# Optimization experiments

Hardware: AMD Instinct MI355X
Metric: run time of the kernel (lower is better)

Reference implementation:

```python
import jax, jax.numpy as jnp
import numpy as np

B, T, D, H = 4, 2048, 1024, 16
HD = D // H

def setup_inputs() -> dict:
    key = jax.random.key(0)
    ks = jax.random.split(key, 7)
    s = 1.0 / np.sqrt(D)
    return {
        "x": jax.random.normal(ks[0], (B, T, D), dtype=jnp.float32),
        "w_qkv": jax.random.uniform(ks[1], (D, 3 * D), jnp.float32, -s, s),
        "b_qkv": jax.random.uniform(ks[2], (3 * D,), jnp.float32, -s, s),
        "w_proj": jax.random.uniform(ks[3], (D, D), jnp.float32, -s, s),
        "b_proj": jax.random.uniform(ks[4], (D,), jnp.float32, -s, s),
        "ln_gamma": jnp.ones((D,), jnp.float32),
        "ln_beta": jnp.zeros((D,), jnp.float32),
    }

def reference(x, w_qkv, b_qkv, w_proj, b_proj, ln_gamma, ln_beta):
    eps = 1e-5
    scale = HD ** -0.5
    residual = x
    # Pre-norm LayerNorm over last dim
    mu = jnp.mean(x, axis=-1, keepdims=True)
    var = jnp.mean(jnp.square(x - mu), axis=-1, keepdims=True)
    xn = (x - mu) * jax.lax.rsqrt(var + eps) * ln_gamma + ln_beta
    # QKV projection: (B,T,3D) -> (3,B,H,T,HD)
    qkv = xn @ w_qkv + b_qkv
    qkv = qkv.reshape(B, T, 3, H, HD).transpose(2, 0, 3, 1, 4)
    q, k, v = qkv[0], qkv[1], qkv[2]
    # Scaled dot-product attention (full T x T scores, as in source)
    attn = jnp.einsum('bhqd,bhkd->bhqk', q, k) * scale
    attn = jax.nn.softmax(attn, axis=-1)
    out = jnp.einsum('bhqk,bhkd->bhqd', attn, v)
    out = out.transpose(0, 2, 1, 3).reshape(B, T, D)
    out = out @ w_proj + b_proj
    return residual + out
```

## Files before the change

kernel.cpp:

```cpp
#include <hip/hip_runtime.h>
#include <cstdint>
#include <cstddef>

#define B_ 4
#define T_ 2048
#define D_ 1024
#define H_ 16

typedef __attribute__((ext_vector_type(8))) short short8;
typedef __attribute__((ext_vector_type(4))) float f32x4;
typedef __attribute__((ext_vector_type(8))) unsigned short u16x8;

__device__ __forceinline__ unsigned short f2b16(float f) {
  union { float f; unsigned int u; } un; un.f = f;
  unsigned int r = un.u + 0x7fffu + ((un.u >> 16) & 1u);
  return (unsigned short)(r >> 16);
}
__device__ __forceinline__ void async_cp16(const void* g, void* l) {
  __builtin_amdgcn_global_load_lds((const __attribute__((address_space(1))) void*)g,
                                   (__attribute__((address_space(3))) void*)l,
                                   16, 0, 0);
}
__device__ __forceinline__ f32x4 mfma16(short8 a, short8 b, f32x4 c) {
  return __builtin_amdgcn_mfma_f32_16x16x32_bf16(a, b, c, 0, 0, 0);
}

__global__ __launch_bounds__(256) void prep_kernel(const float* __restrict__ x,
                                                   const float* __restrict__ gamma,
                                                   const float* __restrict__ beta,
                                                   unsigned short* __restrict__ xn,
                                                   const float* __restrict__ wq,
                                                   unsigned short* __restrict__ wTq,
                                                   const float* __restrict__ wp,
                                                   unsigned short* __restrict__ wTp) {
  __shared__ float sh[8];
  __shared__ float tile[32][33];
  const int bid = blockIdx.x;
  const int t = threadIdx.x;

  if (bid < 8192) {
    const int row = bid;
    const float4 v = ((const float4*)(x + (size_t)row * D_))[t];
    float s  = v.x + v.y + v.z + v.w;
    float s2 = v.x*v.x + v.y*v.y + v.z*v.z + v.w*v.w;
    #pragma unroll
    for (int off = 32; off > 0; off >>= 1) {
      s  += __shfl_down(s, off);
      s2 += __shfl_down(s2, off);
    }
    const int wv = t >> 6, lane = t & 63;
    if (lane == 0) { sh[wv] = s; sh[4 + wv] = s2; }
    __syncthreads();
    if (t == 0) {
      float ts  = sh[0] + sh[1] + sh[2] + sh[3];
      float ts2 = sh[4] + sh[5] + sh[6] + sh[7];
      float mu  = ts * (1.0f / D_);
      float var = ts2 * (1.0f / D_) - mu * mu;
      sh[0] = mu;
      sh[1] = rsqrtf(var + 1e-5f);
    }
    __syncthreads();
    const float mu = sh[0], rs = sh[1];
    const float4 g  = ((const float4*)gamma)[t];
    const float4 bb = ((const float4*)beta)[t];
    ushort4 o;
    o.x = f2b16((v.x - mu) * rs * g.x + bb.x);
    o.y = f2b16((v.y - mu) * rs * g.y + bb.y);
    o.z = f2b16((v.z - mu) * rs * g.z + bb.z);
    o.w = f2b16((v.w - mu) * rs * g.w + bb.w);
    ((ushort4*)(xn + (size_t)row * D_))[t] = o;
  } else {
    const float* w; unsigned short* wT; int K, N, bx, by;
    if (bid < 8192 + 3072) {
      const int idx = bid - 8192;
      w = wq; wT = wTq; K = 1024; N = 3072; bx = idx % 96; by = idx / 96;
    } else {
      const int idx = bid - 11264;
      w = wp; wT = wTp; K = 1024; N = 1024; bx = idx % 32; by = idx / 32;
    }
    const int n0 = bx * 32, k0 = by * 32;
    const int tx = t & 31, ty = t >> 5;
    #pragma unroll
    for (int i = 0; i < 32; i += 8)
      tile[ty + i][tx] = w[(size_t)(k0 + ty + i) * N + n0 + tx];
    __syncthreads();
    #pragma unroll
    for (int i = 0; i < 32; i += 8)
      wT[(size_t)(n0 + ty + i) * K + k0 + tx] = f2b16(tile[tx][ty + i]);
  }
}

__global__ __launch_bounds__(512, 2) void gemm256_qkv(const unsigned short* __restrict__ A,
                                                      const unsigned short* __restrict__ Bt,
                                                      const float* __restrict__ bias,
                                                      unsigned short* __restrict__ qB,
                                                      unsigned short* __restrict__ kB,
                                                      unsigned short* __restrict__ vtB) {
  constexpr int K = 1024;
  constexpr int NT = K / 64;
  __shared__ __align__(16) unsigned short As[32768];
  __shared__ __align__(16) unsigned short Bs[32768];

  const int tid  = threadIdx.x;
  const int lane = tid & 63;
  const int wv   = tid >> 6;
  const int l15  = lane & 15, quad = lane >> 4;
  const int wr   = wv >> 1;
  const int wc   = wv & 1;

  const int w = (blockIdx.x & 7) * 48 + (blockIdx.x >> 3);
  const int tileM = (w & 31) * 256;
  const int tileN = (w >> 5) * 256;

  const int sr  = tid >> 3;
  const int scs = ((tid & 7) ^ (sr & 7)) * 8;
  const unsigned short* gA = A  + (size_t)(tileM + sr) * K + scs;
  const unsigned short* gB = Bt + (size_t)(tileN + sr) * K + scs;

  auto stageA = [&](int h, int ko, int wbuf) {
    const unsigned short* g = gA + (size_t)(h * 128) * K + ko;
    unsigned short* l = &As[wbuf * 16384 + h * 8192 + tid * 8];
    async_cp16(g, l);
    async_cp16(g + (size_t)64 * K, l + 4096);
  };
  auto stageB = [&](int h, int ko, int wbuf) {
    const unsigned short* g = gB + (size_t)(h * 128) * K + ko;
    unsigned short* l = &Bs[wbuf * 16384 + h * 8192 + tid * 8];
    async_cp16(g, l);
    async_cp16(g + (size_t)64 * K, l + 4096);
  };

  const int rA  = wr * 32 + l15;
  const int rB  = wc * 64 + l15;
  const int ck0 = ((0 + quad) ^ (l15 & 7)) * 8;
  const int ck1 = ((4 + quad) ^ (l15 & 7)) * 8;

  f32x4 acc[2][2][2][4] = {};

#define MFMA16(QM, QN, AF, BF)                                                          \
  do {                                                                                  \
    _Pragma("unroll") for (int fm = 0; fm < 2; ++fm)                                    \
    _Pragma("unroll") for (int fn = 0; fn < 4; ++fn) {                                  \
      acc[QM][QN][fm][fn] = mfma16(AF[fm][0], BF[fn][0], acc[QM][QN][fm][fn]);          \
      acc[QM][QN][fm][fn] = mfma16(AF[fm][1], BF[fn][1], acc[QM][QN][fm][fn]);          \
    }                                                                                   \
  } while (0)

  stageA(0, 0, 0);
  stageB(0, 0, 0);
  stageB(1, 0, 0);
  stageA(1, 0, 0);
  asm volatile("s_waitcnt vmcnt(4)" ::: "memory");
  asm volatile("s_barrier" ::: "memory");

  #pragma unroll 2
  for (int kt = 0; kt < NT; ++kt) {
    const int buf = kt & 1;
    const unsigned short* Ab = &As[buf * 16384];
    const unsigned short* Bb = &Bs[buf * 16384];
    const int wbuf = buf ^ 1;
    const bool st = (kt + 1) < NT;
    const int ko = (kt + 1) * 64;

    short8 a[2][2], b0[4][2], b1[4][2];

    #pragma unroll
    for (int fm = 0; fm < 2; ++fm) {
      a[fm][0] = *(const short8*)&Ab[(rA + fm * 16) * 64 + ck0];
      a[fm][1] = *(const short8*)&Ab[(rA + fm * 16) * 64 + ck1];
    }
    #pragma unroll
    for (int fn = 0; fn < 4; ++fn) {
      b0[fn][0] = *(const short8*)&Bb[(rB + fn * 16) * 64 + ck0];
      b0[fn][1] = *(const short8*)&Bb[(rB + fn * 16) * 64 + ck1];
    }
    if (st) stageA(0, ko, wbuf);
    asm volatile("s_waitcnt lgkmcnt(0)" ::: "memory");
    __builtin_amdgcn_sched_barrier(0);
    __builtin_amdgcn_s_setprio(1);
    MFMA16(0, 0, a, b0);
    __builtin_amdgcn_s_setprio(0);
    if (st) asm volatile("s_waitcnt vmcnt(4)" ::: "memory");
    else    asm volatile("s_waitcnt vmcnt(2)" ::: "memory");
    asm volatile("s_barrier" ::: "memory");

    #pragma unroll
    for (int fn = 0; fn < 4; ++fn) {
      b1[fn][0] = *(const short8*)&Bb[8192 + (rB + fn * 16) * 64 + ck0];
      b1[fn][1] = *(const short8*)&Bb[8192 + (rB + fn * 16) * 64 + ck1];
    }
    if (st) stageB(0, ko, wbuf);
    asm volatile("s_waitcnt lgkmcnt(0)" ::: "memory");
    __builtin_amdgcn_sched_barrier(0);
    __builtin_amdgcn_s_setprio(1);
    MFMA16(0, 1, a, b1);
    __builtin_amdgcn_s_setprio(0);
    if (st) asm volatile("s_waitcnt vmcnt(4)" ::: "memory");
    else    asm volatile("s_waitcnt vmcnt(0)" ::: "memory");
    asm volatile("s_barrier" ::: "memory");

    #pragma unroll
    for (int fm = 0; fm < 2; ++fm) {
      a[fm][0] = *(const short8*)&Ab[8192 + (rA + fm * 16) * 64 + ck0];
      a[fm][1] = *(const short8*)&Ab[8192 + (rA + fm * 16) * 64 + ck1];
    }
    if (st) stageB(1, ko, wbuf);
    asm volatile("s_waitcnt lgkmcnt(0)" ::: "memory");
    __builtin_amdgcn_sched_barrier(0);
    __builtin_amdgcn_s_setprio(1);
    MFMA16(1, 0, a, b0);
    __builtin_amdgcn_s_setprio(0);
    asm volatile("s_barrier" ::: "memory");

    if (st) stageA(1, ko, wbuf);
    __builtin_amdgcn_s_setprio(1);
    MFMA16(1, 1, a, b1);
    __builtin_amdgcn_s_setprio(0);
    if (st) asm volatile("s_waitcnt vmcnt(4)" ::: "memory");
    asm volatile("s_barrier" ::: "memory");
  }
#undef MFMA16

  if (tileN < 2048) {
    unsigned short* E = &As[wv * 2304];
    #pragma unroll
    for (int qm = 0; qm < 2; ++qm) {
      #pragma unroll
      for (int qn = 0; qn < 2; ++qn) {
        const int colBase = tileN + qn * 128 + wc * 64;
        const int rowBase = tileM + qm * 128 + wr * 32;
        #pragma unroll
        for (int fn = 0; fn < 4; ++fn) {
          const int col = colBase + fn * 16 + l15;
          const float bv = bias[col];
          const float sc = (col < 1024) ? 0.180336880f : 1.0f;
          #pragma unroll
          for (int fm = 0; fm < 2; ++fm)
            #pragma unroll
            for (int r = 0; r < 4; ++r)
              E[(fm * 16 + quad * 4 + r) * 72 + fn * 16 + l15] =
                  f2b16((acc[qm][qn][fm][fn][r] + bv) * sc);
        }
        const int secq = colBase >> 10;
        const int hh   = (colBase & 1023) >> 6;
        unsigned short* outSec = (secq == 0) ? qB : kB;
        #pragma unroll
        for (int it = 0; it < 4; ++it) {
          const int lrow = it * 8 + (lane >> 3);
          const int row = rowBase + lrow;
          const int b_ = row >> 11, tt = row & 2047;
          const u16x8 val = *(const u16x8*)&E[lrow * 72 + (lane & 7) * 8];
          *(u16x8*)(outSec + ((size_t)(b_ * 16 + hh) * T_ + tt) * 64 + (lane & 7) * 8) = val;
        }
      }
    }
  } else {
    const int b_    = tileM >> 11;
    const int tbase = tileM & 2047;
    const int h0    = (tileN - 2048) >> 6;
    unsigned short* TL = (wr < 2) ? As : Bs;
    const int cpr = 32 * (wr & 1) + 8 * quad;
    #pragma unroll
    for (int qm = 0; qm < 2; ++qm) {
      #pragma unroll
      for (int qn = 0; qn < 2; ++qn) {
        const int head = qn * 2 + wc;
        const int colBase = tileN + qn * 128 + wc * 64;
        #pragma unroll
        for (int fn = 0; fn < 4; ++fn) {
          const int dv = fn * 16 + l15;
          const float bv = bias[colBase + fn * 16 + l15];
          #pragma unroll
          for (int fm = 0; fm < 2; ++fm)
            #pragma unroll
            for (int r = 0; r < 4; ++r)
              TL[head * 4352 + dv * 68 + cpr + 4 * fm + r] =
                  f2b16(acc[qm][qn][fm][fn][r] + bv);
        }
      }
      __syncthreads();
      {
        const unsigned short* SA = (wv < 4) ? As : Bs;
        const int head = wv & 3;
        const int tb   = qm * 2 + (wv >> 2);
        const size_t base = ((size_t)(b_ * 16 + h0 + head) * 64) * T_ + tbase + tb * 64;
        const int c4 = (lane & 15) * 4;
        #pragma unroll
        for (int i = 0; i < 16; ++i) {
          const int dv = i * 4 + (lane >> 4);
          const ushort4 val = *(const ushort4*)&SA[head * 4352 + dv * 68 + c4];
          *(ushort4*)(vtB + base + (size_t)dv * T_ + c4) = val;
        }
      }
      __syncthreads();
    }
  }
}

template <int MODE, int NN>
__global__ __launch_bounds__(512, 2) void gemm8p(const unsigned short* __restrict__ A,
                                                 const unsigned short* __restrict__ Bt,
                                                 const float* __restrict__ bias,
                                                 const float* __restrict__ resid,
                                                 float* __restrict__ outF) {
  constexpr int K = 1024;
  constexpr int NT = 16;
  __shared__ __align__(16) unsigned short As[16384];
  __shared__ __align__(16) unsigned short Bs[32768];

  const int tid  = threadIdx.x;
  const int lane = tid & 63;
  const int wv   = tid >> 6;
  const int l15  = lane & 15, quad = lane >> 4;
  const int wr   = wv >> 1;
  const int wc   = wv & 1;

  constexpr int CPX = (64 * (NN / 256)) / 8;
  const int w = (blockIdx.x & 7) * CPX + (blockIdx.x >> 3);
  const int tileM = (w & 63) * 128;
  const int tileN = (w >> 6) * 256;

  const int sr  = tid >> 3;
  const int scs = ((tid & 7) ^ (sr & 7)) * 8;
  const unsigned short* gA = A  + (size_t)(tileM + sr) * K + scs;
  const unsigned short* gB = Bt + (size_t)(tileN + sr) * K + scs;

  auto stA = [&](int h, int ko, int wb) {
    async_cp16(gA + (size_t)(h * 64) * K + ko, &As[wb * 8192 + h * 4096 + tid * 8]);
  };
  auto stB = [&](int h, int ko, int wb) {
    const unsigned short* g = gB + (size_t)(h * 128) * K + ko;
    unsigned short* l = &Bs[wb * 16384 + h * 8192 + tid * 8];
    async_cp16(g, l);
    async_cp16(g + (size_t)64 * K, l + 4096);
  };

  const int rA  = wr * 16 + l15;
  const int rB  = wc * 64 + l15;
  const int ck0 = ((0 + quad) ^ (l15 & 7)) * 8;
  const int ck1 = ((4 + quad) ^ (l15 & 7)) * 8;

  f32x4 acc[2][2][4] = {};

  stA(0, 0, 0); stB(0, 0, 0); stB(1, 0, 0); stA(1, 0, 0);
  asm volatile("s_waitcnt vmcnt(3)" ::: "memory");
  asm volatile("s_barrier" ::: "memory");

  #pragma unroll 2
  for (int kt = 0; kt < NT; ++kt) {
    const int buf = kt & 1;
    const unsigned short* Ab = &As[buf * 8192];
    const unsigned short* Bb = &Bs[buf * 16384];
    const int wb = buf ^ 1;
    const bool st = (kt + 1) < NT;
    const int ko = (kt + 1) * 64;

    short8 a[2], b0[4][2], b1[4][2];

    a[0] = *(const short8*)&Ab[rA * 64 + ck0];
    a[1] = *(const short8*)&Ab[rA * 64 + ck1];
    #pragma unroll
    for (int fn = 0; fn < 4; ++fn) {
      b0[fn][0] = *(const short8*)&Bb[(rB + fn * 16) * 64 + ck0];
      b0[fn][1] = *(const short8*)&Bb[(rB + fn * 16) * 64 + ck1];
    }
    if (st) stA(0, ko, wb);
    asm volatile("s_waitcnt lgkmcnt(0)" ::: "memory");
    __builtin_amdgcn_sched_barrier(0);
    __builtin_amdgcn_s_setprio(1);
    #pragma unroll
    for (int fn = 0; fn < 4; ++fn) {
      acc[0][0][fn] = mfma16(a[0], b0[fn][0], acc[0][0][fn]);
      acc[0][0][fn] = mfma16(a[1], b0[fn][1], acc[0][0][fn]);
    }
    __builtin_amdgcn_s_setprio(0);
    if (st) asm volatile("s_waitcnt vmcnt(2)" ::: "memory");
    else    asm volatile("s_waitcnt vmcnt(1)" ::: "memory");
    asm volatile("s_barrier" ::: "memory");

    #pragma unroll
    for (int fn = 0; fn < 4; ++fn) {
      b1[fn][0] = *(const short8*)&Bb[8192 + (rB + fn * 16) * 64 + ck0];
      b1[fn][1] = *(const short8*)&Bb[8192 + (rB + fn * 16) * 64 + ck1];
    }
    if (st) stB(0, ko, wb);
    asm volatile("s_waitcnt lgkmcnt(0)" ::: "memory");
    __builtin_amdgcn_sched_barrier(0);
    __builtin_amdgcn_s_setprio(1);
    #pragma unroll
    for (int fn = 0; fn < 4; ++fn) {
      acc[0][1][fn] = mfma16(a[0], b1[fn][0], acc[0][1][fn]);
      acc[0][1][fn] = mfma16(a[1], b1[fn][1], acc[0][1][fn]);
    }
    __builtin_amdgcn_s_setprio(0);
    if (st) asm volatile("s_waitcnt vmcnt(3)" ::: "memory");
    else    asm volatile("s_waitcnt vmcnt(0)" ::: "memory");
    asm volatile("s_barrier" ::: "memory");

    a[0] = *(const short8*)&Ab[4096 + rA * 64 + ck0];
    a[1] = *(const short8*)&Ab[4096 + rA * 64 + ck1];
    if (st) stB(1, ko, wb);
    asm volatile("s_waitcnt lgkmcnt(0)" ::: "memory");
    __builtin_amdgcn_sched_barrier(0);
    __builtin_amdgcn_s_setprio(1);
    #pragma unroll
    for (int fn = 0; fn < 4; ++fn) {
      acc[1][0][fn] = mfma16(a[0], b0[fn][0], acc[1][0][fn]);
      acc[1][0][fn] = mfma16(a[1], b0[fn][1], acc[1][0][fn]);
    }
    __builtin_amdgcn_s_setprio(0);
    asm volatile("s_barrier" ::: "memory");

    if (st) stA(1, ko, wb);
    __builtin_amdgcn_s_setprio(1);
    #pragma unroll
    for (int fn = 0; fn < 4; ++fn) {
      acc[1][1][fn] = mfma16(a[0], b1[fn][0], acc[1][1][fn]);
      acc[1][1][fn] = mfma16(a[1], b1[fn][1], acc[1][1][fn]);
    }
    __builtin_amdgcn_s_setprio(0);
    if (st) asm volatile("s_waitcnt vmcnt(3)" ::: "memory");
    asm volatile("s_barrier" ::: "memory");
  }

  #pragma unroll
  for (int qm = 0; qm < 2; ++qm) {
    #pragma unroll
    for (int qn = 0; qn < 2; ++qn) {
      #pragma unroll
      for (int fn = 0; fn < 4; ++fn) {
        const int col = tileN + qn * 128 + wc * 64 + fn * 16 + l15;
        const float bv = bias[col];
        #pragma unroll
        for (int r = 0; r < 4; ++r) {
          const int row = tileM + qm * 64 + wr * 16 + quad * 4 + r;
          const size_t idx = (size_t)row * NN + col;
          outF[idx] = acc[qm][qn][fn][r] + bv + resid[idx];
        }
      }
    }
  }
}

__global__ __launch_bounds__(256, 4) void attn_mfma(const unsigned short* __restrict__ qB,
                                                    const unsigned short* __restrict__ kB,
                                                    const unsigned short* __restrict__ vtB,
                                                    unsigned short* __restrict__ aout) {
  __shared__ unsigned short Ks[2][64 * 64];
  __shared__ unsigned short Vs[2][64 * 64];

  const int tid = threadIdx.x;
  const int bid = blockIdx.x;
  const int bh = bid & 63;
  const int qb = bid >> 6;
  const int b = bh >> 4, h = bh & 15;
  const int wv = tid >> 6, lane = tid & 63;
  const int l15 = lane & 15, quad = lane >> 4;

  const unsigned short* qP = qB  + (size_t)bh * T_ * 64;
  const unsigned short* kP = kB  + (size_t)bh * T_ * 64;
  const unsigned short* vP = vtB + (size_t)bh * 64 * T_;
  const int q0 = qb * 128 + wv * 32;

  short8 qf[2][2];
  #pragma unroll
  for (int mi = 0; mi < 2; ++mi)
    #pragma unroll
    for (int ks = 0; ks < 2; ++ks)
      qf[mi][ks] = *(const short8*)(qP + ((size_t)(q0 + mi * 16 + l15)) * 64 + ks * 32 + quad * 8);

  const short8 onesf = {0x3F80, 0x3F80, 0x3F80, 0x3F80, 0x3F80, 0x3F80, 0x3F80, 0x3F80};
  f32x4 accO[2][5] = {};

  const int lrow  = lane >> 3;
  const int lchnk = (lane & 7) ^ (lrow & 7);
  const size_t kOff0 = (size_t)((wv * 2 + 0) * 8 + lrow) * 64 + lchnk * 8;
  const size_t kOff1 = (size_t)((wv * 2 + 1) * 8 + lrow) * 64 + lchnk * 8;
  const size_t vOff0 = (size_t)((wv * 2 + 0) * 8 + lrow) * T_ + lchnk * 8;
  const size_t vOff1 = (size_t)((wv * 2 + 1) * 8 + lrow) * T_ + lchnk * 8;
  const int lOff0 = (wv * 2 + 0) * 512 + lane * 8;
  const int lOff1 = (wv * 2 + 1) * 512 + lane * 8;

  async_cp16(kP + kOff0, &Ks[0][lOff0]);
  async_cp16(kP + kOff1, &Ks[0][lOff1]);
  async_cp16(vP + vOff0, &Vs[0][lOff0]);
  async_cp16(vP + vOff1, &Vs[0][lOff1]);
  __syncthreads();

  for (int kt = 0; kt < 32; ++kt) {
    const int buf = kt & 1;
    if (kt + 1 < 32) {
      const unsigned short* kg = kP + (size_t)(kt + 1) * 64 * 64;
      const unsigned short* vg = vP + (kt + 1) * 64;
      async_cp16(kg + kOff0, &Ks[buf ^ 1][lOff0]);
      async_cp16(kg + kOff1, &Ks[buf ^ 1][lOff1]);
      async_cp16(vg + vOff0, &Vs[buf ^ 1][lOff0]);
      async_cp16(vg + vOff1, &Vs[buf ^ 1][lOff1]);
    }
    const unsigned short* K_ = Ks[buf];
    const unsigned short* V_ = Vs[buf];

    f32x4 accT[4][2] = {};
    __builtin_amdgcn_s_setprio(1);
    #pragma unroll
    for (int ks = 0; ks < 2; ++ks) {
      #pragma unroll
      for (int cc = 0; cc < 4; ++cc) {
        const short8 kb = *(const short8*)&K_[(cc * 16 + l15) * 64 +
                                              (((ks << 2) | quad) ^ (l15 & 7)) * 8];
        accT[cc][0] = mfma16(kb, qf[0][ks], accT[cc][0]);
        accT[cc][1] = mfma16(kb, qf[1][ks], accT[cc][1]);
      }
    }
    __builtin_amdgcn_s_setprio(0);

    short8 pa[2][2];
    #pragma unroll
    for (int mi = 0; mi < 2; ++mi) {
      #pragma unroll
      for (int ks = 0; ks < 2; ++ks) {
        union { unsigned short u[8]; short8 s; } pk;
        #pragma unroll
        for (int r = 0; r < 4; ++r) {
          union { float f; unsigned int u; } e0, e1;
          e0.f = __builtin_amdgcn_exp2f(accT[2 * ks + 0][mi][r]);
          e1.f = __builtin_amdgcn_exp2f(accT[2 * ks + 1][mi][r]);
          pk.u[r]     = (unsigned short)(e0.u >> 16);
          pk.u[4 + r] = (unsigned short)(e1.u >> 16);
        }
        pa[mi][ks] = pk.s;
      }
    }

    __builtin_amdgcn_s_setprio(1);
    #pragma unroll
    for (int ks = 0; ks < 2; ++ks) {
      short8 vb[4];
      #pragma unroll
      for (int nj = 0; nj < 4; ++nj)
        vb[nj] = *(const short8*)&V_[(nj * 16 + l15) * 64 +
                                     (((ks << 2) | quad) ^ (l15 & 7)) * 8];
      #pragma unroll
      for (int mi = 0; mi < 2; ++mi) {
        #pragma unroll
        for (int nj = 0; nj < 4; ++nj)
          accO[mi][nj] = mfma16(pa[mi][ks], vb[nj], accO[mi][nj]);
        accO[mi][4] = mfma16(pa[mi][ks], onesf, accO[mi][4]);
      }
    }
    __builtin_amdgcn_s_setprio(0);

    __syncthreads();
  }

  #pragma unroll
  for (int mi = 0; mi < 2; ++mi) {
    #pragma unroll
    for (int r = 0; r < 4; ++r) {
      const float inv = 1.0f / accO[mi][4][r];
      const int row = q0 + mi * 16 + quad * 4 + r;
      unsigned short* op = aout + (size_t)(b * T_ + row) * D_ + h * 64 + l15;
      #pragma unroll
      for (int nj = 0; nj < 4; ++nj)
        op[nj * 16] = f2b16(accO[mi][nj][r] * inv);
    }
  }
}

extern "C" void kernel_launch(void* const* d_in, const int* in_sizes, int n_in,
                              void* d_out, int out_size, void* d_ws, size_t ws_size,
                              hipStream_t stream) {
  const float* x      = (const float*)d_in[0];
  const float* w_qkv  = (const float*)d_in[1];
  const float* b_qkv  = (const float*)d_in[2];
  const float* w_proj = (const float*)d_in[3];
  const float* b_proj = (const float*)d_in[4];
  const float* ln_g   = (const float*)d_in[5];
  const float* ln_b   = (const float*)d_in[6];
  float* out = (float*)d_out;

  char* ws = (char*)d_ws;
  unsigned short* xn   = (unsigned short*)(ws);
  unsigned short* wTq  = (unsigned short*)(ws + (size_t)(16 << 20));
  unsigned short* wTp  = (unsigned short*)(ws + (size_t)(22 << 20));
  unsigned short* qBuf = (unsigned short*)(ws + (size_t)(24 << 20));
  unsigned short* kBuf = (unsigned short*)(ws + (size_t)(40 << 20));
  unsigned short* vtB  = (unsigned short*)(ws + (size_t)(72 << 20));
  unsigned short* aout = xn;

  prep_kernel<<<12288, 256, 0, stream>>>(x, ln_g, ln_b, xn, w_qkv, wTq, w_proj, wTp);
  gemm256_qkv<<<384, 512, 0, stream>>>(xn, wTq, b_qkv, qBuf, kBuf, vtB);
  attn_mfma<<<1024, 256, 0, stream>>>(qBuf, kBuf, vtB, aout);
  gemm8p<1, 1024><<<256, 512, 0, stream>>>(aout, wTp, b_proj, x, out);
}
```

Measured before the change: 267.9 us.

## Software-pipeline attention QK^T one tile ahead with triple-buffered K, remap QKV GEMM tiles

The attention kernel now computes QK^T and the exp/pack for the next key tile while running the PV MFMAs on the current one. K moves to a three-slot ring buffer so it can be prefetched two tiles ahead, and V stays double-buffered. The aim is to hide the exp/pack latency and the MFMA dependency chain behind independent work, at the cost of more live registers and extra LDS. The QKV GEMM also changes its block-to-tile mapping so each XCD handles a contiguous group of M tiles, which is meant to improve L2 reuse.

```diff
diff --git a/kernel.cpp b/kernel.cpp
--- a/kernel.cpp
+++ b/kernel.cpp
@@ -108,9 +108,10 @@
   const int wr   = wv >> 1;
   const int wc   = wv & 1;
 
-  const int w = (blockIdx.x & 7) * 48 + (blockIdx.x >> 3);
-  const int tileM = (w & 31) * 256;
-  const int tileN = (w >> 5) * 256;
+  const int xcd = blockIdx.x & 7;
+  const int i   = blockIdx.x >> 3;
+  const int tileM = (xcd * 4 + (i & 3)) * 256;
+  const int tileN = (i >> 2) * 256;
 
   const int sr  = tid >> 3;
   const int scs = ((tid & 7) ^ (sr & 7)) * 8;
@@ -286,8 +287,8 @@
         const size_t base = ((size_t)(b_ * 16 + h0 + head) * 64) * T_ + tbase + tb * 64;
         const int c4 = (lane & 15) * 4;
         #pragma unroll
-        for (int i = 0; i < 16; ++i) {
-          const int dv = i * 4 + (lane >> 4);
+        for (int i2 = 0; i2 < 16; ++i2) {
+          const int dv = i2 * 4 + (lane >> 4);
           const ushort4 val = *(const ushort4*)&SA[head * 4352 + dv * 68 + c4];
           *(ushort4*)(vtB + base + (size_t)dv * T_ + c4) = val;
         }
@@ -446,8 +447,8 @@
                                                     const unsigned short* __restrict__ kB,
                                                     const unsigned short* __restrict__ vtB,
                                                     unsigned short* __restrict__ aout) {
-  __shared__ unsigned short Ks[2][64 * 64];
-  __shared__ unsigned short Vs[2][64 * 64];
+  __shared__ unsigned short Ks[3 * 4096];
+  __shared__ unsigned short Vs[2 * 4096];
 
   const int tid = threadIdx.x;
   const int bid = blockIdx.x;
@@ -471,6 +472,8 @@
 
   const short8 onesf = {0x3F80, 0x3F80, 0x3F80, 0x3F80, 0x3F80, 0x3F80, 0x3F80, 0x3F80};
   f32x4 accO[2][5] = {};
+  f32x4 accT[4][2];
+  short8 pa[2][2];
 
   const int lrow  = lane >> 3;
   const int lchnk = (lane & 7) ^ (lrow & 7);
@@ -481,27 +484,12 @@
   const int lOff0 = (wv * 2 + 0) * 512 + lane * 8;
   const int lOff1 = (wv * 2 + 1) * 512 + lane * 8;
 
-  async_cp16(kP + kOff0, &Ks[0][lOff0]);
-  async_cp16(kP + kOff1, &Ks[0][lOff1]);
-  async_cp16(vP + vOff0, &Vs[0][lOff0]);
-  async_cp16(vP + vOff1, &Vs[0][lOff1]);
-  __syncthreads();
-
-  for (int kt = 0; kt < 32; ++kt) {
-    const int buf = kt & 1;
-    if (kt + 1 < 32) {
-      const unsigned short* kg = kP + (size_t)(kt + 1) * 64 * 64;
-      const unsigned short* vg = vP + (kt + 1) * 64;
-      async_cp16(kg + kOff0, &Ks[buf ^ 1][lOff0]);
-      async_cp16(kg + kOff1, &Ks[buf ^ 1][lOff1]);
-      async_cp16(vg + vOff0, &Vs[buf ^ 1][lOff0]);
-      async_cp16(vg + vOff1, &Vs[buf ^ 1][lOff1]);
-    }
-    const unsigned short* K_ = Ks[buf];
-    const unsigned short* V_ = Vs[buf];
-
-    f32x4 accT[4][2] = {};
-    __builtin_amdgcn_s_setprio(1);
+  auto QKT = [&](const unsigned short* K_) {
+    #pragma unroll
+    for (int cc = 0; cc < 4; ++cc) {
+      accT[cc][0] = f32x4{0.f, 0.f, 0.f, 0.f};
+      accT[cc][1] = f32x4{0.f, 0.f, 0.f, 0.f};
+    }
     #pragma unroll
     for (int ks = 0; ks < 2; ++ks) {
       #pragma unroll
@@ -512,9 +500,8 @@
         accT[cc][1] = mfma16(kb, qf[1][ks], accT[cc][1]);
       }
     }
-    __builtin_amdgcn_s_setprio(0);
-
-    short8 pa[2][2];
+  };
+  auto PACK = [&]() {
     #pragma unroll
     for (int mi = 0; mi < 2; ++mi) {
       #pragma unroll
@@ -531,8 +518,36 @@
         pa[mi][ks] = pk.s;
       }
     }
-
-    __builtin_amdgcn_s_setprio(1);
+  };
+
+  async_cp16(kP + kOff0, &Ks[lOff0]);
+  async_cp16(kP + kOff1, &Ks[lOff1]);
+  async_cp16(vP + vOff0, &Vs[lOff0]);
+  async_cp16(vP + vOff1, &Vs[lOff1]);
+  async_cp16(kP + 4096 + kOff0, &Ks[4096 + lOff0]);
+  async_cp16(kP + 4096 + kOff1, &Ks[4096 + lOff1]);
+  __syncthreads();
+  QKT(&Ks[0]);
+  PACK();
+
+  int kq = 1;
+  int kd = 2;
+  for (int kt = 0; kt < 32; ++kt) {
+    if (kt < 30) {
+      const unsigned short* kg = kP + (size_t)(kt + 2) * 4096;
+      async_cp16(kg + kOff0, &Ks[kd * 4096 + lOff0]);
+      async_cp16(kg + kOff1, &Ks[kd * 4096 + lOff1]);
+    }
+    if (kt < 31) {
+      const unsigned short* vg = vP + (kt + 1) * 64;
+      async_cp16(vg + vOff0, &Vs[((kt + 1) & 1) * 4096 + lOff0]);
+      async_cp16(vg + vOff1, &Vs[((kt + 1) & 1) * 4096 + lOff1]);
+    }
+    const unsigned short* V_ = &Vs[(kt & 1) * 4096];
+
+    __builtin_amdgcn_s_setprio(1);
+    if (kt < 31) QKT(&Ks[kq * 4096]);
+
     #pragma unroll
     for (int ks = 0; ks < 2; ++ks) {
       short8 vb[4];
@@ -550,7 +565,12 @@
     }
     __builtin_amdgcn_s_setprio(0);
 
+    if (kt < 31) PACK();
+
     __syncthreads();
+    const int kn = 3 - kq - kd;
+    kq = kd;
+    kd = kn;
   }
 
   #pragma unroll
```

Measured after the change: 256.6 us. 4.2% less time.
